# Performance work log

Hardware: AMD Instinct MI355X
Metric: run time of the kernel (lower is better)

## Reference

```python
import jax, jax.numpy as jnp
import numpy as np

N_NODES = 50000
N_EDGES = 600000
IN_CH = 300
HID = 128
N_CLASSES = 2
N_GRAPHS = 128
BN_EPS = 1e-5


def setup_inputs() -> dict:
    key = jax.random.key(0)
    ks = jax.random.split(key, 24)
    x = jax.random.normal(ks[0], (N_NODES, IN_CH), dtype=jnp.float32)
    edge_index = jax.random.randint(ks[1], (2, N_EDGES), 0, N_NODES, dtype=jnp.int64)
    batch = jnp.sort(jax.random.randint(ks[2], (N_NODES,), 0, N_GRAPHS, dtype=jnp.int64))

    def glorot(k, shape):
        fan_in, fan_out = shape
        s = jnp.sqrt(2.0 / (fan_in + fan_out)).astype(jnp.float32)
        return jax.random.normal(k, shape, dtype=jnp.float32) * s

    inp = {"x": x, "edge_index": edge_index, "batch": batch}
    # SAGEConv params: W_l (neighbor branch), W_r (root branch), bias
    dims = [(IN_CH, HID), (HID, HID), (HID, HID)]
    for i, (din, dout) in enumerate(dims, start=1):
        inp[f"W{i}l"] = glorot(ks[3 * i], (din, dout))
        inp[f"W{i}r"] = glorot(ks[3 * i + 1], (din, dout))
        inp[f"b{i}"] = jnp.zeros((dout,), dtype=jnp.float32)
        inp[f"g{i}"] = jnp.ones((dout,), dtype=jnp.float32)   # BN gamma
        inp[f"be{i}"] = jnp.zeros((dout,), dtype=jnp.float32)  # BN beta
    inp["Wc"] = glorot(ks[20], (HID, N_CLASSES))
    inp["bc"] = jnp.zeros((N_CLASSES,), dtype=jnp.float32)
    return inp


def _sage_conv(x, src, dst, Wl, Wr, b):
    # mean-aggregate neighbor features (messages flow src -> dst)
    msg_sum = jax.ops.segment_sum(x[src], dst, num_segments=N_NODES)
    deg = jax.ops.segment_sum(jnp.ones((src.shape[0],), dtype=x.dtype), dst,
                              num_segments=N_NODES)
    mean = msg_sum / jnp.maximum(deg, 1.0)[:, None]
    return mean @ Wl + x @ Wr + b


def _bn_relu(h, gamma, beta):
    mu = jnp.mean(h, axis=0)
    var = jnp.var(h, axis=0)
    h = (h - mu) * jax.lax.rsqrt(var + BN_EPS) * gamma + beta
    return jax.nn.relu(h)


def reference(x, edge_index, batch,
              W1l, W1r, b1, g1, be1,
              W2l, W2r, b2, g2, be2,
              W3l, W3r, b3, g3, be3,
              Wc, bc):
    src, dst = edge_index[0], edge_index[1]
    h = _bn_relu(_sage_conv(x, src, dst, W1l, W1r, b1), g1, be1)
    h = _bn_relu(_sage_conv(h, src, dst, W2l, W2r, b2), g2, be2)
    h = _bn_relu(_sage_conv(h, src, dst, W3l, W3r, b3), g3, be3)
    # global mean pool per graph
    pooled = jax.ops.segment_sum(h, batch, num_segments=N_GRAPHS)
    cnt = jax.ops.segment_sum(jnp.ones((h.shape[0],), dtype=h.dtype), batch,
                              num_segments=N_GRAPHS)
    hg = pooled / jnp.maximum(cnt, 1.0)[:, None]
    out = hg @ Wc + bc
    return out, hg
```

## Files before the change

kernel.cpp:

```cpp
#include <hip/hip_runtime.h>

#define N_NODES   50000
#define N_EDGES   600000
#define IN_CH     300
#define HID       128
#define N_CLASSES 2
#define N_GRAPHS  128
#define BN_EPS    1e-5f

#define NB ((N_NODES + 511) / 512)
#define KP1 320
#define NREP 32
#define DEGB ((N_EDGES + 255) / 256)

typedef __attribute__((ext_vector_type(8))) short bf8_t;
typedef __attribute__((ext_vector_type(4))) float f4_t;

__device__ __forceinline__ unsigned short f2bf(float x) {
    union { float f; unsigned u; } q; q.f = x;
    unsigned r = q.u + 0x7fffu + ((q.u >> 16) & 1u);
    return (unsigned short)(r >> 16);
}
__device__ __forceinline__ float bf2f(unsigned short h) {
    union { float f; unsigned u; } q; q.u = ((unsigned)h) << 16; return q.f;
}

__global__ __launch_bounds__(256) void deg_prepw(const int* __restrict__ dst,
                                                 int* __restrict__ ideg,
                                                 const float* __restrict__ W1l,
                                                 const float* __restrict__ W1r,
                                                 const float* __restrict__ W2l,
                                                 const float* __restrict__ W2r,
                                                 const float* __restrict__ W3l,
                                                 const float* __restrict__ W3r,
                                                 unsigned short* __restrict__ B1h,
                                                 unsigned short* __restrict__ B1l,
                                                 unsigned short* __restrict__ B2h,
                                                 unsigned short* __restrict__ B2l,
                                                 unsigned short* __restrict__ B3h,
                                                 unsigned short* __restrict__ B3l) {
    int b = blockIdx.x;
    if (b < DEGB) {
        int e = b * 256 + threadIdx.x;
        if (e < N_EDGES) atomicAdd(&ideg[dst[e]], 1);
        return;
    }
    int pb = b - DEGB;
    int layer, base;
    if (pb < 320)      { layer = 0; base = pb; }
    else if (pb < 448) { layer = 1; base = pb - 320; }
    else               { layer = 2; base = pb - 448; }
    int Kp = (layer == 0) ? KP1 : HID;
    int K  = (layer == 0) ? IN_CH : HID;
    const float* Wl = (layer == 0) ? W1l : ((layer == 1) ? W2l : W3l);
    const float* Wr = (layer == 0) ? W1r : ((layer == 1) ? W2r : W3r);
    unsigned short* Bh = (layer == 0) ? B1h : ((layer == 1) ? B2h : B3h);
    unsigned short* Bl = (layer == 0) ? B1l : ((layer == 1) ? B2l : B3l);
    int idx = base * 256 + threadIdx.x;
    int n = idx / Kp;
    int k = idx - n * Kp;
    float v = 0.f;
    if (k < K) v = (n < 128) ? Wl[k * 128 + n] : Wr[k * 128 + (n - 128)];
    unsigned short h = f2bf(v);
    unsigned short l = f2bf(v - bf2f(h));
    int NST   = Kp >> 5;
    int ntile = n >> 4;
    int l16n  = n & 15;
    int kstep = k >> 5;
    int kk    = k & 31;
    int lane2 = (kk >> 3) * 16 + l16n;
    int addr  = ((ntile * NST + kstep) * 64 + lane2) * 8 + (kk & 7);
    Bh[addr] = h;
    Bl[addr] = l;
}

__global__ __launch_bounds__(256) void scan_fused(const int* __restrict__ ideg,
                                                  int* __restrict__ row_start,
                                                  float* __restrict__ invdeg,
                                                  int* __restrict__ bsum,
                                                  int* __restrict__ bflag) {
    int b = blockIdx.x, t = threadIdx.x;
    int lane = t & 63, wv = t >> 6;
    int i0 = b * 512 + t * 2;
    int v0 = 0, v1 = 0;
    if (i0 < N_NODES) {
        int2 v = *(const int2*)&ideg[i0];
        v0 = v.x; v1 = v.y;
    }
    int tot = v0 + v1;
    int s = tot;
#pragma unroll
    for (int d = 1; d < 64; d <<= 1) {
        int u = __shfl_up(s, d);
        if (lane >= d) s += u;
    }
    __shared__ int ws[4];
    if (lane == 63) ws[wv] = s;
    __syncthreads();
    int btot = ws[0] + ws[1] + ws[2] + ws[3];
    if (t == 0) {
        atomicExch(&bsum[b], btot);
        __threadfence();
        atomicExch(&bflag[b], 1);
    }
    int part = 0;
    if (t < b) {
        while (atomicAdd(&bflag[t], 0) == 0) {}
        part = atomicAdd(&bsum[t], 0);
    }
#pragma unroll
    for (int d = 1; d < 64; d <<= 1) part += __shfl_down(part, d);
    __shared__ int ps[4];
    if (lane == 0) ps[wv] = part;
    __syncthreads();
    int boff = ps[0] + ps[1] + ps[2] + ps[3];
    int woff = 0;
    for (int w = 0; w < wv; ++w) woff += ws[w];
    int base = boff + woff + (s - tot);
    if (i0 < N_NODES) {
        row_start[i0]     = base;
        row_start[i0 + 1] = base + v0;
        invdeg[i0]     = 1.0f / fmaxf((float)v0, 1.0f);
        invdeg[i0 + 1] = 1.0f / fmaxf((float)v1, 1.0f);
    }
    if (t == 0 && b == NB - 1) row_start[N_NODES] = boff + btot;
}

__global__ __launch_bounds__(256) void fill_kernel(const int* __restrict__ src,
                                                   const int* __restrict__ dst,
                                                   const int* __restrict__ row_start,
                                                   int* __restrict__ cursor,
                                                   int* __restrict__ csr_src) {
    int e = blockIdx.x * 256 + threadIdx.x;
    if (e >= N_EDGES) return;
    int d = dst[e];
    int pos = row_start[d] + atomicAdd(&cursor[d], 1);
    csr_src[pos] = src[e];
}

__global__ __launch_bounds__(256) void gemm_mfma_x(const float* __restrict__ X,
                                                   int M,
                                                   const unsigned short* __restrict__ Bhi,
                                                   const unsigned short* __restrict__ Blo,
                                                   const float* __restrict__ bias,
                                                   unsigned short* __restrict__ C0,
                                                   float* __restrict__ C1) {
    __shared__ __align__(16) unsigned short sAh[2][64 * 32];
    __shared__ __align__(16) unsigned short sAl[2][64 * 32];

    const int tid  = threadIdx.x;
    const int lane = tid & 63;
    const int wave = tid >> 6;
    const int l16  = lane & 15;
    const int quad = lane >> 4;
    const long m0  = (long)blockIdx.x * 64;
    const int  n0  = wave * 64;

    f4_t acc[4][4];
#pragma unroll
    for (int mt = 0; mt < 4; ++mt)
#pragma unroll
        for (int nt = 0; nt < 4; ++nt) acc[mt][nt] = (f4_t){0.f, 0.f, 0.f, 0.f};

    const int ar  = tid >> 2;
    const int cl  = tid & 3;
    const int cpa = cl ^ ((ar >> 1) & 3);
    long agr = m0 + ar;
    if (agr >= M) agr = M - 1;
    const float* gX = X + agr * IN_CH;

    const int rsw = (quad ^ ((l16 >> 1) & 3)) * 8;
    const int NT  = KP1 / 32;

    const bf8_t* Bh0 = (const bf8_t*)Bhi;
    const bf8_t* Bl0 = (const bf8_t*)Blo;

    auto loadA = [&](int k0, float4& a0, float4& a1) {
        int gk = k0 + cl * 8;
        a0 = (gk + 4 <= IN_CH) ? *(const float4*)(gX + gk)
                               : make_float4(0.f, 0.f, 0.f, 0.f);
        a1 = (gk + 8 <= IN_CH) ? *(const float4*)(gX + gk + 4)
                               : make_float4(0.f, 0.f, 0.f, 0.f);
    };
    auto storeA = [&](int buf, float4 a0, float4 a1) {
        float f[8];
        f[0] = a0.x; f[1] = a0.y; f[2] = a0.z; f[3] = a0.w;
        f[4] = a1.x; f[5] = a1.y; f[6] = a1.z; f[7] = a1.w;
        bf8_t h8, l8;
#pragma unroll
        for (int j = 0; j < 8; ++j) {
            unsigned short h = f2bf(f[j]);
            h8[j] = (short)h;
            l8[j] = (short)f2bf(f[j] - bf2f(h));
        }
        *(bf8_t*)&sAh[buf][ar * 32 + cpa * 8] = h8;
        *(bf8_t*)&sAl[buf][ar * 32 + cpa * 8] = l8;
    };
    auto loadB = [&](int t, bf8_t (&bh)[4], bf8_t (&bl)[4]) {
#pragma unroll
        for (int nt = 0; nt < 4; ++nt) {
            long bi = ((long)(wave * 4 + nt) * NT + t) * 64 + lane;
            bh[nt] = Bh0[bi];
            bl[nt] = Bl0[bi];
        }
    };

    bf8_t bhv[4], blv[4];
    {
        float4 a0, a1;
        loadA(0, a0, a1);
        loadB(0, bhv, blv);
        storeA(0, a0, a1);
    }
    __syncthreads();

    int cur = 0;
    for (int t = 0; t < NT; ++t) {
        float4 na0 = make_float4(0.f, 0.f, 0.f, 0.f);
        float4 na1 = make_float4(0.f, 0.f, 0.f, 0.f);
        bf8_t nbh[4], nbl[4];
        const bool more = (t + 1 < NT);
        if (more) {
            loadA((t + 1) * 32, na0, na1);
            loadB(t + 1, nbh, nbl);
        }

        bf8_t ah[4], al[4];
#pragma unroll
        for (int mt = 0; mt < 4; ++mt) {
            ah[mt] = *(const bf8_t*)&sAh[cur][(mt * 16 + l16) * 32 + rsw];
            al[mt] = *(const bf8_t*)&sAl[cur][(mt * 16 + l16) * 32 + rsw];
        }
#pragma unroll
        for (int nt = 0; nt < 4; ++nt)
#pragma unroll
            for (int mt = 0; mt < 4; ++mt)
                acc[mt][nt] = __builtin_amdgcn_mfma_f32_16x16x32_bf16(ah[mt], bhv[nt], acc[mt][nt], 0, 0, 0);
#pragma unroll
        for (int nt = 0; nt < 4; ++nt)
#pragma unroll
            for (int mt = 0; mt < 4; ++mt)
                acc[mt][nt] = __builtin_amdgcn_mfma_f32_16x16x32_bf16(al[mt], bhv[nt], acc[mt][nt], 0, 0, 0);
#pragma unroll
        for (int nt = 0; nt < 4; ++nt)
#pragma unroll
            for (int mt = 0; mt < 4; ++mt)
                acc[mt][nt] = __builtin_amdgcn_mfma_f32_16x16x32_bf16(ah[mt], blv[nt], acc[mt][nt], 0, 0, 0);

        if (more) {
            storeA(cur ^ 1, na0, na1);
#pragma unroll
            for (int nt = 0; nt < 4; ++nt) {
                bhv[nt] = nbh[nt];
                blv[nt] = nbl[nt];
            }
        }
        __syncthreads();
        cur ^= 1;
    }

    const bool left = (n0 < 128);
    if (left) {
        int ncol[4];
#pragma unroll
        for (int nt = 0; nt < 4; ++nt) ncol[nt] = n0 + nt * 16 + l16;
#pragma unroll
        for (int mt = 0; mt < 4; ++mt)
#pragma unroll
            for (int r = 0; r < 4; ++r) {
                long row = m0 + mt * 16 + quad * 4 + r;
                if (row < M) {
#pragma unroll
                    for (int nt = 0; nt < 4; ++nt)
                        C0[row * 128 + ncol[nt]] = f2bf(acc[mt][nt][r]);
                }
            }
    } else {
        float badd[4];
        int   ncol[4];
#pragma unroll
        for (int nt = 0; nt < 4; ++nt) {
            int ng = n0 + nt * 16 + l16 - 128;
            ncol[nt] = ng;
            badd[nt] = bias[ng];
        }
#pragma unroll
        for (int mt = 0; mt < 4; ++mt)
#pragma unroll
            for (int r = 0; r < 4; ++r) {
                long row = m0 + mt * 16 + quad * 4 + r;
                if (row < M) {
#pragma unroll
                    for (int nt = 0; nt < 4; ++nt)
                        C1[row * 128 + ncol[nt]] = acc[mt][nt][r] + badd[nt];
                }
            }
    }
}

__global__ __launch_bounds__(256) void gemm_mfma_h(const float* __restrict__ Hpre,
                                                   int M,
                                                   const float* __restrict__ rep,
                                                   const float* __restrict__ gamma,
                                                   const float* __restrict__ beta,
                                                   const unsigned short* __restrict__ Bhi,
                                                   const unsigned short* __restrict__ Blo,
                                                   const float* __restrict__ bias,
                                                   unsigned short* __restrict__ C0,
                                                   float* __restrict__ C1) {
    __shared__ __align__(16) unsigned short sAh[2][64 * 32];
    __shared__ __align__(16) unsigned short sAl[2][64 * 32];
    __shared__ float sSC[256];

    const int tid  = threadIdx.x;
    const int lane = tid & 63;
    const int wave = tid >> 6;
    const int l16  = lane & 15;
    const int quad = lane >> 4;
    const long m0  = (long)blockIdx.x * 64;
    const int  n0  = wave * 64;

    {
        float* S = (float*)sAh;
        float a = 0.f;
#pragma unroll
        for (int r = 0; r < NREP; ++r) a += rep[r * 256 + tid];
        S[tid] = a;
        __syncthreads();
        if (tid < HID) {
            const float invn = 1.0f / (float)N_NODES;
            float mu  = S[tid] * invn;
            float var = S[HID + tid] * invn - mu * mu;
            float sc  = gamma[tid] * rsqrtf(var + BN_EPS);
            sSC[tid]       = sc;
            sSC[HID + tid] = beta[tid] - mu * sc;
        }
        __syncthreads();
    }

    f4_t acc[4][4];
#pragma unroll
    for (int mt = 0; mt < 4; ++mt)
#pragma unroll
        for (int nt = 0; nt < 4; ++nt) acc[mt][nt] = (f4_t){0.f, 0.f, 0.f, 0.f};

    const int ar  = tid >> 2;
    const int cl  = tid & 3;
    const int cpa = cl ^ ((ar >> 1) & 3);
    long agr = m0 + ar;
    if (agr >= M) agr = M - 1;
    const float* gH = Hpre + agr * HID;

    const int rsw = (quad ^ ((l16 >> 1) & 3)) * 8;
    const int NT  = HID / 32;

    const bf8_t* Bh0 = (const bf8_t*)Bhi;
    const bf8_t* Bl0 = (const bf8_t*)Blo;

    auto loadA = [&](int k0, float4& a0, float4& a1) {
        int gk = k0 + cl * 8;
        a0 = *(const float4*)(gH + gk);
        a1 = *(const float4*)(gH + gk + 4);
    };
    auto storeA = [&](int buf, int k0, float4 v0, float4 v1) {
        const int gk = k0 + cl * 8;
        float4 s0 = *(const float4*)&sSC[gk];
        float4 s1 = *(const float4*)&sSC[gk + 4];
        float4 t0 = *(const float4*)&sSC[HID + gk];
        float4 t1 = *(const float4*)&sSC[HID + gk + 4];
        float f[8];
        f[0] = fmaxf(v0.x * s0.x + t0.x, 0.f);
        f[1] = fmaxf(v0.y * s0.y + t0.y, 0.f);
        f[2] = fmaxf(v0.z * s0.z + t0.z, 0.f);
        f[3] = fmaxf(v0.w * s0.w + t0.w, 0.f);
        f[4] = fmaxf(v1.x * s1.x + t1.x, 0.f);
        f[5] = fmaxf(v1.y * s1.y + t1.y, 0.f);
        f[6] = fmaxf(v1.z * s1.z + t1.z, 0.f);
        f[7] = fmaxf(v1.w * s1.w + t1.w, 0.f);
        bf8_t h8, l8;
#pragma unroll
        for (int j = 0; j < 8; ++j) {
            unsigned short h = f2bf(f[j]);
            h8[j] = (short)h;
            l8[j] = (short)f2bf(f[j] - bf2f(h));
        }
        *(bf8_t*)&sAh[buf][ar * 32 + cpa * 8] = h8;
        *(bf8_t*)&sAl[buf][ar * 32 + cpa * 8] = l8;
    };
    auto loadB = [&](int t, bf8_t (&bh)[4], bf8_t (&bl)[4]) {
#pragma unroll
        for (int nt = 0; nt < 4; ++nt) {
            long bi = ((long)(wave * 4 + nt) * NT + t) * 64 + lane;
            bh[nt] = Bh0[bi];
            bl[nt] = Bl0[bi];
        }
    };

    bf8_t bhv[4], blv[4];
    {
        float4 a0, a1;
        loadA(0, a0, a1);
        loadB(0, bhv, blv);
        storeA(0, 0, a0, a1);
    }
    __syncthreads();

    int cur = 0;
#pragma unroll
    for (int t = 0; t < 4; ++t) {
        float4 na0 = make_float4(0.f, 0.f, 0.f, 0.f);
        float4 na1 = make_float4(0.f, 0.f, 0.f, 0.f);
        bf8_t nbh[4], nbl[4];
        const bool more = (t < 3);
        if (more) {
            loadA((t + 1) * 32, na0, na1);
            loadB(t + 1, nbh, nbl);
        }

        bf8_t ah[4], al[4];
#pragma unroll
        for (int mt = 0; mt < 4; ++mt) {
            ah[mt] = *(const bf8_t*)&sAh[cur][(mt * 16 + l16) * 32 + rsw];
            al[mt] = *(const bf8_t*)&sAl[cur][(mt * 16 + l16) * 32 + rsw];
        }
#pragma unroll
        for (int nt = 0; nt < 4; ++nt)
#pragma unroll
            for (int mt = 0; mt < 4; ++mt)
                acc[mt][nt] = __builtin_amdgcn_mfma_f32_16x16x32_bf16(ah[mt], bhv[nt], acc[mt][nt], 0, 0, 0);
#pragma unroll
        for (int nt = 0; nt < 4; ++nt)
#pragma unroll
            for (int mt = 0; mt < 4; ++mt)
                acc[mt][nt] = __builtin_amdgcn_mfma_f32_16x16x32_bf16(al[mt], bhv[nt], acc[mt][nt], 0, 0, 0);
#pragma unroll
        for (int nt = 0; nt < 4; ++nt)
#pragma unroll
            for (int mt = 0; mt < 4; ++mt)
                acc[mt][nt] = __builtin_amdgcn_mfma_f32_16x16x32_bf16(ah[mt], blv[nt], acc[mt][nt], 0, 0, 0);

        if (more) {
            storeA(cur ^ 1, (t + 1) * 32, na0, na1);
#pragma unroll
            for (int nt = 0; nt < 4; ++nt) {
                bhv[nt] = nbh[nt];
                blv[nt] = nbl[nt];
            }
        }
        __syncthreads();
        cur ^= 1;
    }

    const bool left = (n0 < 128);
    if (left) {
        int ncol[4];
#pragma unroll
        for (int nt = 0; nt < 4; ++nt) ncol[nt] = n0 + nt * 16 + l16;
#pragma unroll
        for (int mt = 0; mt < 4; ++mt)
#pragma unroll
            for (int r = 0; r < 4; ++r) {
                long row = m0 + mt * 16 + quad * 4 + r;
                if (row < M) {
#pragma unroll
                    for (int nt = 0; nt < 4; ++nt)
                        C0[row * 128 + ncol[nt]] = f2bf(acc[mt][nt][r]);
                }
            }
    } else {
        float badd[4];
        int   ncol[4];
#pragma unroll
        for (int nt = 0; nt < 4; ++nt) {
            int ng = n0 + nt * 16 + l16 - 128;
            ncol[nt] = ng;
            badd[nt] = bias[ng];
        }
#pragma unroll
        for (int mt = 0; mt < 4; ++mt)
#pragma unroll
            for (int r = 0; r < 4; ++r) {
                long row = m0 + mt * 16 + quad * 4 + r;
                if (row < M) {
#pragma unroll
                    for (int nt = 0; nt < 4; ++nt)
                        C1[row * 128 + ncol[nt]] = acc[mt][nt][r] + badd[nt];
                }
            }
    }
}

__global__ __launch_bounds__(256) void gather_agg(const unsigned short* __restrict__ Pl,
                                                  const int* __restrict__ row_start,
                                                  const int* __restrict__ csr_src,
                                                  const float* __restrict__ invdeg,
                                                  float* __restrict__ out,
                                                  float* __restrict__ rep) {
    int slot = threadIdx.x >> 5;
    int lane = threadIdx.x & 31;
    int node = blockIdx.x * 8 + slot;
    int beg = row_start[node];
    int end = row_start[node + 1];
    const unsigned short* base = Pl + lane * 4;
    float sx = 0.f, sy = 0.f, sz = 0.f, sw = 0.f;
    int j = beg;
    int deg = end - beg;

    if (deg > 0) {
        int n16 = (deg < 16) ? deg : 16;
        int idx[16];
#pragma unroll
        for (int u = 0; u < 16; ++u)
            idx[u] = csr_src[(u < n16) ? (j + u) : j];
        ushort4 v[16];
#pragma unroll
        for (int u = 0; u < 16; ++u)
            v[u] = *(const ushort4*)(base + (long)idx[u] * HID);
#pragma unroll
        for (int u = 0; u < 16; ++u) {
            float m = (u < n16) ? 1.f : 0.f;
            sx += m * bf2f(v[u].x); sy += m * bf2f(v[u].y);
            sz += m * bf2f(v[u].z); sw += m * bf2f(v[u].w);
        }
        j += n16;
    }
    for (; j + 8 <= end; j += 8) {
        int idx[8];
#pragma unroll
        for (int u = 0; u < 8; ++u) idx[u] = csr_src[j + u];
        ushort4 v[8];
#pragma unroll
        for (int u = 0; u < 8; ++u) v[u] = *(const ushort4*)(base + (long)idx[u] * HID);
#pragma unroll
        for (int u = 0; u < 8; ++u) {
            sx += bf2f(v[u].x); sy += bf2f(v[u].y);
            sz += bf2f(v[u].z); sw += bf2f(v[u].w);
        }
    }
    if (j + 4 <= end) {
        int idx[4];
#pragma unroll
        for (int u = 0; u < 4; ++u) idx[u] = csr_src[j + u];
        ushort4 v[4];
#pragma unroll
        for (int u = 0; u < 4; ++u) v[u] = *(const ushort4*)(base + (long)idx[u] * HID);
#pragma unroll
        for (int u = 0; u < 4; ++u) {
            sx += bf2f(v[u].x); sy += bf2f(v[u].y);
            sz += bf2f(v[u].z); sw += bf2f(v[u].w);
        }
        j += 4;
    }
    for (; j < end; ++j) {
        int i0 = csr_src[j];
        ushort4 v0 = *(const ushort4*)(base + (long)i0 * HID);
        sx += bf2f(v0.x); sy += bf2f(v0.y); sz += bf2f(v0.z); sw += bf2f(v0.w);
    }
    float w = invdeg[node];
    float* o = out + (long)node * HID + lane * 4;
    float4 cur = *(float4*)o;
    cur.x += sx * w;
    cur.y += sy * w;
    cur.z += sz * w;
    cur.w += sw * w;
    *(float4*)o = cur;

    __shared__ float red[8][HID];
    float* repb = rep + (blockIdx.x & (NREP - 1)) * 256;
    *(float4*)&red[slot][lane * 4] = make_float4(cur.x, cur.y, cur.z, cur.w);
    __syncthreads();
    if (threadIdx.x < HID) {
        float tsum = 0.f;
#pragma unroll
        for (int s = 0; s < 8; ++s) tsum += red[s][threadIdx.x];
        atomicAdd(&repb[threadIdx.x], tsum);
    }
    __syncthreads();
    *(float4*)&red[slot][lane * 4] = make_float4(cur.x * cur.x, cur.y * cur.y,
                                                 cur.z * cur.z, cur.w * cur.w);
    __syncthreads();
    if (threadIdx.x < HID) {
        float tsum = 0.f;
#pragma unroll
        for (int s = 0; s < 8; ++s) tsum += red[s][threadIdx.x];
        atomicAdd(&repb[HID + threadIdx.x], tsum);
    }
}

__global__ __launch_bounds__(1024) void poolhead_bn(const float* __restrict__ h,
                                                    const int* __restrict__ batch,
                                                    const float* __restrict__ rep,
                                                    const float* __restrict__ gamma,
                                                    const float* __restrict__ beta,
                                                    const float* __restrict__ Wc,
                                                    const float* __restrict__ bc,
                                                    float* __restrict__ out) {
    __shared__ float S[256];
    __shared__ float SC[256];
    int g = blockIdx.x;
    int t = threadIdx.x;
    int c = t & 127;
    int half = t >> 7;
    if (t < 256) {
        float a = 0.f;
#pragma unroll
        for (int r = 0; r < NREP; ++r) a += rep[r * 256 + t];
        S[t] = a;
    }
    __shared__ int lo_sh, hi_sh;
    if (t == 0) {
        int lo = 0, hi = N_NODES;
        while (lo < hi) { int m = (lo + hi) >> 1; if (batch[m] < g) lo = m + 1; else hi = m; }
        lo_sh = lo;
        int lo2 = lo, hi2 = N_NODES;
        while (lo2 < hi2) { int m = (lo2 + hi2) >> 1; if (batch[m] < g + 1) lo2 = m + 1; else hi2 = m; }
        hi_sh = lo2;
    }
    __syncthreads();
    if (t < HID) {
        const float invn = 1.0f / (float)N_NODES;
        float mu  = S[t] * invn;
        float var = S[HID + t] * invn - mu * mu;
        float sc  = gamma[t] * rsqrtf(var + BN_EPS);
        SC[t]       = sc;
        SC[HID + t] = beta[t] - mu * sc;
    }
    __syncthreads();
    float bsc = SC[c], bsh = SC[HID + c];
    int lo = lo_sh, hi = hi_sh;
    float a0 = 0.f, a1 = 0.f, a2 = 0.f, a3 = 0.f;
    int r = lo + half;
    for (; r + 24 < hi; r += 32) {
        a0 += fmaxf(h[(long)(r +  0) * HID + c] * bsc + bsh, 0.f);
        a1 += fmaxf(h[(long)(r +  8) * HID + c] * bsc + bsh, 0.f);
        a2 += fmaxf(h[(long)(r + 16) * HID + c] * bsc + bsh, 0.f);
        a3 += fmaxf(h[(long)(r + 24) * HID + c] * bsc + bsh, 0.f);
    }
    for (; r < hi; r += 8) a0 += fmaxf(h[(long)r * HID + c] * bsc + bsh, 0.f);
    __shared__ float red[8][HID];
    red[half][c] = (a0 + a1) + (a2 + a3);
    __syncthreads();
    __shared__ float r0[HID], r1[HID];
    if (t < HID) {
        float inv = 1.0f / fmaxf((float)(hi - lo), 1.0f);
        float v = 0.f;
#pragma unroll
        for (int s = 0; s < 8; ++s) v += red[s][t];
        v *= inv;
        out[N_GRAPHS * N_CLASSES + g * HID + t] = v;
        r0[t] = v * Wc[t * 2 + 0];
        r1[t] = v * Wc[t * 2 + 1];
    }
    __syncthreads();
    if (t < 2) {
        const float* rr = t ? r1 : r0;
        float sum = bc[t];
        for (int i = 0; i < HID; ++i) sum += rr[i];
        out[g * 2 + t] = sum;
    }
}

extern "C" void kernel_launch(void* const* d_in, const int* in_sizes, int n_in,
                              void* d_out, int out_size, void* d_ws, size_t ws_size,
                              hipStream_t stream) {
    const float* x     = (const float*)d_in[0];
    const int*   ei    = (const int*)d_in[1];
    const int*   batch = (const int*)d_in[2];
    const float* W1l = (const float*)d_in[3];
    const float* W1r = (const float*)d_in[4];
    const float* b1  = (const float*)d_in[5];
    const float* g1  = (const float*)d_in[6];
    const float* be1 = (const float*)d_in[7];
    const float* W2l = (const float*)d_in[8];
    const float* W2r = (const float*)d_in[9];
    const float* b2  = (const float*)d_in[10];
    const float* g2  = (const float*)d_in[11];
    const float* be2 = (const float*)d_in[12];
    const float* W3l = (const float*)d_in[13];
    const float* W3r = (const float*)d_in[14];
    const float* b3  = (const float*)d_in[15];
    const float* g3  = (const float*)d_in[16];
    const float* be3 = (const float*)d_in[17];
    const float* Wc  = (const float*)d_in[18];
    const float* bc  = (const float*)d_in[19];

    const int* src = ei;
    const int* dst = ei + N_EDGES;

    float* ws = (float*)d_ws;
    const long FEAT = (long)N_NODES * HID;
    unsigned short* Pl16 = (unsigned short*)ws;
    float* buf1 = ws + FEAT;
    float* buf2 = ws + 2 * FEAT;
    int*   ideg      = (int*)(ws + 3 * FEAT);
    int*   cursor    = ideg + N_NODES;
    int*   bsum      = cursor + N_NODES;
    int*   bflag     = bsum + 128;
    int*   row_start = bflag + 128;
    int*   csr_src   = row_start + N_NODES + 4;
    float* invdeg    = (float*)(csr_src + N_EDGES);
    float* reps      = invdeg + N_NODES;
    unsigned short* B1h = (unsigned short*)(reps + 3 * NREP * 256);
    unsigned short* B1l = B1h + 256 * KP1;
    unsigned short* B2h = B1l + 256 * KP1;
    unsigned short* B2l = B2h + 256 * HID;
    unsigned short* B3h = B2l + 256 * HID;
    unsigned short* B3l = B3h + 256 * HID;

    float* outp = (float*)d_out;

    const int gemm_grid   = (N_NODES + 63) / 64;
    const int gather_grid = N_NODES / 8;
    const int dp_grid     = DEGB + 320 + 128 + 128;

    hipMemsetAsync(ideg, 0, (2 * N_NODES + 256) * sizeof(int), stream);
    hipMemsetAsync(reps, 0, 3 * NREP * 256 * sizeof(float), stream);

    deg_prepw<<<dp_grid, 256, 0, stream>>>(dst, ideg, W1l, W1r, W2l, W2r, W3l, W3r,
                                           B1h, B1l, B2h, B2l, B3h, B3l);
    scan_fused<<<NB, 256, 0, stream>>>(ideg, row_start, invdeg, bsum, bflag);
    fill_kernel<<<(N_EDGES + 255) / 256, 256, 0, stream>>>(src, dst, row_start, cursor, csr_src);

    gemm_mfma_x<<<gemm_grid, 256, 0, stream>>>(x, N_NODES, B1h, B1l, b1, Pl16, buf1);
    gather_agg<<<gather_grid, 256, 0, stream>>>(Pl16, row_start, csr_src, invdeg, buf1, reps);

    gemm_mfma_h<<<gemm_grid, 256, 0, stream>>>(buf1, N_NODES, reps, g1, be1,
                                               B2h, B2l, b2, Pl16, buf2);
    gather_agg<<<gather_grid, 256, 0, stream>>>(Pl16, row_start, csr_src, invdeg, buf2, reps + NREP * 256);

    gemm_mfma_h<<<gemm_grid, 256, 0, stream>>>(buf2, N_NODES, reps + NREP * 256, g2, be2,
                                               B3h, B3l, b3, Pl16, buf1);
    gather_agg<<<gather_grid, 256, 0, stream>>>(Pl16, row_start, csr_src, invdeg, buf1, reps + 2 * NREP * 256);

    poolhead_bn<<<N_GRAPHS, 1024, 0, stream>>>(buf1, batch, reps + 2 * NREP * 256,
                                               g3, be3, Wc, bc, outp);
}
```

Measured before the change: 371.1 us.

## Stage full A tile in LDS upfront and halve row tile for first GEMM

Both MFMA GEMM kernels now load and convert the entire K extent of their A row tile into shared memory in one up-front phase, replacing the per-K-step double-buffered load/convert/sync pipeline. The loop then only prefetches B fragments and issues MFMAs, with no barriers inside it. The x-input GEMM also shrinks its row tile from 64 to 32 rows, doubling its grid, to keep LDS usage modest and add parallelism. The cost is that global loads no longer overlap with compute inside a block. Overlap now has to come from other resident blocks, and the 32-row tile halves B reuse per block.

Measured after the change: 374.4 us. Within noise of the previous version (+0.9%).

```diff
diff --git a/kernel.cpp b/kernel.cpp
--- a/kernel.cpp
+++ b/kernel.cpp
@@ -145,57 +145,67 @@
                                                    const float* __restrict__ bias,
                                                    unsigned short* __restrict__ C0,
                                                    float* __restrict__ C1) {
-    __shared__ __align__(16) unsigned short sAh[2][64 * 32];
-    __shared__ __align__(16) unsigned short sAl[2][64 * 32];
+    __shared__ __align__(16) unsigned short sAh[10 * 1024];
+    __shared__ __align__(16) unsigned short sAl[10 * 1024];
 
     const int tid  = threadIdx.x;
     const int lane = tid & 63;
     const int wave = tid >> 6;
     const int l16  = lane & 15;
     const int quad = lane >> 4;
-    const long m0  = (long)blockIdx.x * 64;
+    const long m0  = (long)blockIdx.x * 32;
     const int  n0  = wave * 64;
 
-    f4_t acc[4][4];
-#pragma unroll
-    for (int mt = 0; mt < 4; ++mt)
+    f4_t acc[2][4];
+#pragma unroll
+    for (int mt = 0; mt < 2; ++mt)
 #pragma unroll
         for (int nt = 0; nt < 4; ++nt) acc[mt][nt] = (f4_t){0.f, 0.f, 0.f, 0.f};
 
-    const int ar  = tid >> 2;
-    const int cl  = tid & 3;
-    const int cpa = cl ^ ((ar >> 1) & 3);
-    long agr = m0 + ar;
-    if (agr >= M) agr = M - 1;
-    const float* gX = X + agr * IN_CH;
+    {
+        const int ar  = tid >> 3;
+        const int sub = tid & 7;
+        long agr = m0 + ar;
+        if (agr >= M) agr = M - 1;
+        const float* gX = X + agr * IN_CH;
+        const int swm = (ar >> 1) & 3;
+        float4 va[5][2];
+#pragma unroll
+        for (int i = 0; i < 5; ++i) {
+            int c  = sub + 8 * i;
+            int gk = c * 8;
+            va[i][0] = (gk + 4 <= IN_CH) ? *(const float4*)(gX + gk)
+                                         : make_float4(0.f, 0.f, 0.f, 0.f);
+            va[i][1] = (gk + 8 <= IN_CH) ? *(const float4*)(gX + gk + 4)
+                                         : make_float4(0.f, 0.f, 0.f, 0.f);
+        }
+#pragma unroll
+        for (int i = 0; i < 5; ++i) {
+            int c     = sub + 8 * i;
+            int kstep = c >> 2;
+            int cpa   = (c & 3) ^ swm;
+            float f[8];
+            f[0] = va[i][0].x; f[1] = va[i][0].y; f[2] = va[i][0].z; f[3] = va[i][0].w;
+            f[4] = va[i][1].x; f[5] = va[i][1].y; f[6] = va[i][1].z; f[7] = va[i][1].w;
+            bf8_t h8, l8;
+#pragma unroll
+            for (int j = 0; j < 8; ++j) {
+                unsigned short h = f2bf(f[j]);
+                h8[j] = (short)h;
+                l8[j] = (short)f2bf(f[j] - bf2f(h));
+            }
+            int idx = kstep * 1024 + ar * 32 + cpa * 8;
+            *(bf8_t*)&sAh[idx] = h8;
+            *(bf8_t*)&sAl[idx] = l8;
+        }
+    }
+    __syncthreads();
 
     const int rsw = (quad ^ ((l16 >> 1) & 3)) * 8;
     const int NT  = KP1 / 32;
-
     const bf8_t* Bh0 = (const bf8_t*)Bhi;
     const bf8_t* Bl0 = (const bf8_t*)Blo;
 
-    auto loadA = [&](int k0, float4& a0, float4& a1) {
-        int gk = k0 + cl * 8;
-        a0 = (gk + 4 <= IN_CH) ? *(const float4*)(gX + gk)
-                               : make_float4(0.f, 0.f, 0.f, 0.f);
-        a1 = (gk + 8 <= IN_CH) ? *(const float4*)(gX + gk + 4)
-                               : make_float4(0.f, 0.f, 0.f, 0.f);
-    };
-    auto storeA = [&](int buf, float4 a0, float4 a1) {
-        float f[8];
-        f[0] = a0.x; f[1] = a0.y; f[2] = a0.z; f[3] = a0.w;
-        f[4] = a1.x; f[5] = a1.y; f[6] = a1.z; f[7] = a1.w;
-        bf8_t h8, l8;
-#pragma unroll
-        for (int j = 0; j < 8; ++j) {
-            unsigned short h = f2bf(f[j]);
-            h8[j] = (short)h;
-            l8[j] = (short)f2bf(f[j] - bf2f(h));
-        }
-        *(bf8_t*)&sAh[buf][ar * 32 + cpa * 8] = h8;
-        *(bf8_t*)&sAl[buf][ar * 32 + cpa * 8] = l8;
-    };
     auto loadB = [&](int t, bf8_t (&bh)[4], bf8_t (&bl)[4]) {
 #pragma unroll
         for (int nt = 0; nt < 4; ++nt) {
@@ -206,57 +216,42 @@
     };
 
     bf8_t bhv[4], blv[4];
-    {
-        float4 a0, a1;
-        loadA(0, a0, a1);
-        loadB(0, bhv, blv);
-        storeA(0, a0, a1);
-    }
-    __syncthreads();
-
-    int cur = 0;
+    loadB(0, bhv, blv);
     for (int t = 0; t < NT; ++t) {
-        float4 na0 = make_float4(0.f, 0.f, 0.f, 0.f);
-        float4 na1 = make_float4(0.f, 0.f, 0.f, 0.f);
         bf8_t nbh[4], nbl[4];
         const bool more = (t + 1 < NT);
+        if (more) loadB(t + 1, nbh, nbl);
+
+        bf8_t ah[2], al[2];
+#pragma unroll
+        for (int mt = 0; mt < 2; ++mt) {
+            int idx = t * 1024 + (mt * 16 + l16) * 32 + rsw;
+            ah[mt] = *(const bf8_t*)&sAh[idx];
+            al[mt] = *(const bf8_t*)&sAl[idx];
+        }
+#pragma unroll
+        for (int nt = 0; nt < 4; ++nt)
+#pragma unroll
+            for (int mt = 0; mt < 2; ++mt)
+                acc[mt][nt] = __builtin_amdgcn_mfma_f32_16x16x32_bf16(ah[mt], bhv[nt], acc[mt][nt], 0, 0, 0);
+#pragma unroll
+        for (int nt = 0; nt < 4; ++nt)
+#pragma unroll
+            for (int mt = 0; mt < 2; ++mt)
+                acc[mt][nt] = __builtin_amdgcn_mfma_f32_16x16x32_bf16(al[mt], bhv[nt], acc[mt][nt], 0, 0, 0);
+#pragma unroll
+        for (int nt = 0; nt < 4; ++nt)
+#pragma unroll
+            for (int mt = 0; mt < 2; ++mt)
+                acc[mt][nt] = __builtin_amdgcn_mfma_f32_16x16x32_bf16(ah[mt], blv[nt], acc[mt][nt], 0, 0, 0);
+
         if (more) {
-            loadA((t + 1) * 32, na0, na1);
-            loadB(t + 1, nbh, nbl);
-        }
-
-        bf8_t ah[4], al[4];
-#pragma unroll
-        for (int mt = 0; mt < 4; ++mt) {
-            ah[mt] = *(const bf8_t*)&sAh[cur][(mt * 16 + l16) * 32 + rsw];
-            al[mt] = *(const bf8_t*)&sAl[cur][(mt * 16 + l16) * 32 + rsw];
-        }
-#pragma unroll
-        for (int nt = 0; nt < 4; ++nt)
-#pragma unroll
-            for (int mt = 0; mt < 4; ++mt)
-                acc[mt][nt] = __builtin_amdgcn_mfma_f32_16x16x32_bf16(ah[mt], bhv[nt], acc[mt][nt], 0, 0, 0);
-#pragma unroll
-        for (int nt = 0; nt < 4; ++nt)
-#pragma unroll
-            for (int mt = 0; mt < 4; ++mt)
-                acc[mt][nt] = __builtin_amdgcn_mfma_f32_16x16x32_bf16(al[mt], bhv[nt], acc[mt][nt], 0, 0, 0);
-#pragma unroll
-        for (int nt = 0; nt < 4; ++nt)
-#pragma unroll
-            for (int mt = 0; mt < 4; ++mt)
-                acc[mt][nt] = __builtin_amdgcn_mfma_f32_16x16x32_bf16(ah[mt], blv[nt], acc[mt][nt], 0, 0, 0);
-
-        if (more) {
-            storeA(cur ^ 1, na0, na1);
 #pragma unroll
             for (int nt = 0; nt < 4; ++nt) {
                 bhv[nt] = nbh[nt];
                 blv[nt] = nbl[nt];
             }
         }
-        __syncthreads();
-        cur ^= 1;
     }
 
     const bool left = (n0 < 128);
@@ -265,7 +260,7 @@
 #pragma unroll
         for (int nt = 0; nt < 4; ++nt) ncol[nt] = n0 + nt * 16 + l16;
 #pragma unroll
-        for (int mt = 0; mt < 4; ++mt)
+        for (int mt = 0; mt < 2; ++mt)
 #pragma unroll
             for (int r = 0; r < 4; ++r) {
                 long row = m0 + mt * 16 + quad * 4 + r;
@@ -285,7 +280,7 @@
             badd[nt] = bias[ng];
         }
 #pragma unroll
-        for (int mt = 0; mt < 4; ++mt)
+        for (int mt = 0; mt < 2; ++mt)
 #pragma unroll
             for (int r = 0; r < 4; ++r) {
                 long row = m0 + mt * 16 + quad * 4 + r;
@@ -308,8 +303,8 @@
                                                    const float* __restrict__ bias,
                                                    unsigned short* __restrict__ C0,
                                                    float* __restrict__ C1) {
-    __shared__ __align__(16) unsigned short sAh[2][64 * 32];
-    __shared__ __align__(16) unsigned short sAl[2][64 * 32];
+    __shared__ __align__(16) unsigned short sAh[4 * 2048];
+    __shared__ __align__(16) unsigned short sAl[4 * 2048];
     __shared__ float sSC[256];
 
     const int tid  = threadIdx.x;
@@ -344,49 +339,58 @@
 #pragma unroll
         for (int nt = 0; nt < 4; ++nt) acc[mt][nt] = (f4_t){0.f, 0.f, 0.f, 0.f};
 
-    const int ar  = tid >> 2;
-    const int cl  = tid & 3;
-    const int cpa = cl ^ ((ar >> 1) & 3);
-    long agr = m0 + ar;
-    if (agr >= M) agr = M - 1;
-    const float* gH = Hpre + agr * HID;
+    {
+        const int ar = tid >> 2;
+        const int cl = tid & 3;
+        long agr = m0 + ar;
+        if (agr >= M) agr = M - 1;
+        const float* gH = Hpre + agr * HID;
+        const int swm = (ar >> 1) & 3;
+        float4 va[4][2];
+#pragma unroll
+        for (int i = 0; i < 4; ++i) {
+            int gk = (cl + 4 * i) * 8;
+            va[i][0] = *(const float4*)(gH + gk);
+            va[i][1] = *(const float4*)(gH + gk + 4);
+        }
+#pragma unroll
+        for (int i = 0; i < 4; ++i) {
+            int c     = cl + 4 * i;
+            int kstep = c >> 2;
+            int cpa   = (c & 3) ^ swm;
+            int gk    = c * 8;
+            float4 s0 = *(const float4*)&sSC[gk];
+            float4 s1 = *(const float4*)&sSC[gk + 4];
+            float4 t0 = *(const float4*)&sSC[HID + gk];
+            float4 t1 = *(const float4*)&sSC[HID + gk + 4];
+            float f[8];
+            f[0] = fmaxf(va[i][0].x * s0.x + t0.x, 0.f);
+            f[1] = fmaxf(va[i][0].y * s0.y + t0.y, 0.f);
+            f[2] = fmaxf(va[i][0].z * s0.z + t0.z, 0.f);
+            f[3] = fmaxf(va[i][0].w * s0.w + t0.w, 0.f);
+            f[4] = fmaxf(va[i][1].x * s1.x + t1.x, 0.f);
+            f[5] = fmaxf(va[i][1].y * s1.y + t1.y, 0.f);
+            f[6] = fmaxf(va[i][1].z * s1.z + t1.z, 0.f);
+            f[7] = fmaxf(va[i][1].w * s1.w + t1.w, 0.f);
+            bf8_t h8, l8;
+#pragma unroll
+            for (int j = 0; j < 8; ++j) {
+                unsigned short h = f2bf(f[j]);
+                h8[j] = (short)h;
+                l8[j] = (short)f2bf(f[j] - bf2f(h));
+            }
+            int idx = kstep * 2048 + ar * 32 + cpa * 8;
+            *(bf8_t*)&sAh[idx] = h8;
+            *(bf8_t*)&sAl[idx] = l8;
+        }
+    }
+    __syncthreads();
 
     const int rsw = (quad ^ ((l16 >> 1) & 3)) * 8;
     const int NT  = HID / 32;
-
     const bf8_t* Bh0 = (const bf8_t*)Bhi;
     const bf8_t* Bl0 = (const bf8_t*)Blo;
 
-    auto loadA = [&](int k0, float4& a0, float4& a1) {
-        int gk = k0 + cl * 8;
-        a0 = *(const float4*)(gH + gk);
-        a1 = *(const float4*)(gH + gk + 4);
-    };
-    auto storeA = [&](int buf, int k0, float4 v0, float4 v1) {
-        const int gk = k0 + cl * 8;
-        float4 s0 = *(const float4*)&sSC[gk];
-        float4 s1 = *(const float4*)&sSC[gk + 4];
-        float4 t0 = *(const float4*)&sSC[HID + gk];
-        float4 t1 = *(const float4*)&sSC[HID + gk + 4];
-        float f[8];
-        f[0] = fmaxf(v0.x * s0.x + t0.x, 0.f);
-        f[1] = fmaxf(v0.y * s0.y + t0.y, 0.f);
-        f[2] = fmaxf(v0.z * s0.z + t0.z, 0.f);
-        f[3] = fmaxf(v0.w * s0.w + t0.w, 0.f);
-        f[4] = fmaxf(v1.x * s1.x + t1.x, 0.f);
-        f[5] = fmaxf(v1.y * s1.y + t1.y, 0.f);
-        f[6] = fmaxf(v1.z * s1.z + t1.z, 0.f);
-        f[7] = fmaxf(v1.w * s1.w + t1.w, 0.f);
-        bf8_t h8, l8;
-#pragma unroll
-        for (int j = 0; j < 8; ++j) {
-            unsigned short h = f2bf(f[j]);
-            h8[j] = (short)h;
-            l8[j] = (short)f2bf(f[j] - bf2f(h));
-        }
-        *(bf8_t*)&sAh[buf][ar * 32 + cpa * 8] = h8;
-        *(bf8_t*)&sAl[buf][ar * 32 + cpa * 8] = l8;
-    };
     auto loadB = [&](int t, bf8_t (&bh)[4], bf8_t (&bl)[4]) {
 #pragma unroll
         for (int nt = 0; nt < 4; ++nt) {
@@ -397,31 +401,19 @@
     };
 
     bf8_t bhv[4], blv[4];
-    {
-        float4 a0, a1;
-        loadA(0, a0, a1);
-        loadB(0, bhv, blv);
-        storeA(0, 0, a0, a1);
-    }
-    __syncthreads();
-
-    int cur = 0;
+    loadB(0, bhv, blv);
 #pragma unroll
     for (int t = 0; t < 4; ++t) {
-        float4 na0 = make_float4(0.f, 0.f, 0.f, 0.f);
-        float4 na1 = make_float4(0.f, 0.f, 0.f, 0.f);
         bf8_t nbh[4], nbl[4];
         const bool more = (t < 3);
-        if (more) {
-            loadA((t + 1) * 32, na0, na1);
-            loadB(t + 1, nbh, nbl);
-        }
+        if (more) loadB(t + 1, nbh, nbl);
 
         bf8_t ah[4], al[4];
 #pragma unroll
         for (int mt = 0; mt < 4; ++mt) {
-            ah[mt] = *(const bf8_t*)&sAh[cur][(mt * 16 + l16) * 32 + rsw];
-            al[mt] = *(const bf8_t*)&sAl[cur][(mt * 16 + l16) * 32 + rsw];
+            int idx = t * 2048 + (mt * 16 + l16) * 32 + rsw;
+            ah[mt] = *(const bf8_t*)&sAh[idx];
+            al[mt] = *(const bf8_t*)&sAl[idx];
         }
 #pragma unroll
         for (int nt = 0; nt < 4; ++nt)
@@ -440,15 +432,12 @@
                 acc[mt][nt] = __builtin_amdgcn_mfma_f32_16x16x32_bf16(ah[mt], blv[nt], acc[mt][nt], 0, 0, 0);
 
         if (more) {
-            storeA(cur ^ 1, (t + 1) * 32, na0, na1);
 #pragma unroll
             for (int nt = 0; nt < 4; ++nt) {
                 bhv[nt] = nbh[nt];
                 blv[nt] = nbl[nt];
             }
         }
-        __syncthreads();
-        cur ^= 1;
     }
 
     const bool left = (n0 < 128);
@@ -709,7 +698,8 @@
 
     float* outp = (float*)d_out;
 
-    const int gemm_grid   = (N_NODES + 63) / 64;
+    const int gemmx_grid  = (N_NODES + 31) / 32;
+    const int gemmh_grid  = (N_NODES + 63) / 64;
     const int gather_grid = N_NODES / 8;
     const int dp_grid     = DEGB + 320 + 128 + 128;
 
@@ -721,15 +711,15 @@
     scan_fused<<<NB, 256, 0, stream>>>(ideg, row_start, invdeg, bsum, bflag);
     fill_kernel<<<(N_EDGES + 255) / 256, 256, 0, stream>>>(src, dst, row_start, cursor, csr_src);
 
-    gemm_mfma_x<<<gemm_grid, 256, 0, stream>>>(x, N_NODES, B1h, B1l, b1, Pl16, buf1);
+    gemm_mfma_x<<<gemmx_grid, 256, 0, stream>>>(x, N_NODES, B1h, B1l, b1, Pl16, buf1);
     gather_agg<<<gather_grid, 256, 0, stream>>>(Pl16, row_start, csr_src, invdeg, buf1, reps);
 
-    gemm_mfma_h<<<gemm_grid, 256, 0, stream>>>(buf1, N_NODES, reps, g1, be1,
-                                               B2h, B2l, b2, Pl16, buf2);
+    gemm_mfma_h<<<gemmh_grid, 256, 0, stream>>>(buf1, N_NODES, reps, g1, be1,
+                                                B2h, B2l, b2, Pl16, buf2);
     gather_agg<<<gather_grid, 256, 0, stream>>>(Pl16, row_start, csr_src, invdeg, buf2, reps + NREP * 256);
 
-    gemm_mfma_h<<<gemm_grid, 256, 0, stream>>>(buf2, N_NODES, reps + NREP * 256, g2, be2,
-                                               B3h, B3l, b3, Pl16, buf1);
+    gemm_mfma_h<<<gemmh_grid, 256, 0, stream>>>(buf2, N_NODES, reps + NREP * 256, g2, be2,
+                                                B3h, B3l, b3, Pl16, buf1);
     gather_agg<<<gather_grid, 256, 0, stream>>>(Pl16, row_start, csr_src, invdeg, buf1, reps + 2 * NREP * 256);
 
     poolhead_bn<<<N_GRAPHS, 1024, 0, stream>>>(buf1, batch, reps + 2 * NREP * 256,
```

## Fuse CSR fill into first GEMM launch and merge BN stat reductions

Applied to the files above, without the earlier changes.

Appends the edge-to-CSR fill blocks to the layer-1 GEMM grid, so the fill runs concurrently with the GEMM instead of as its own launch. Also computes sum and sum-of-squares in a single shared-memory reduction pass in gather_agg, which drops two barriers and one shared write. The fused kernel carries the GEMM's shared-memory footprint for the fill blocks too, which may limit occupancy for those blocks.

Result: faster. 356.6 us (median of 3 runs) (-3.9%).

```diff
diff --git a/kernel.cpp b/kernel.cpp
--- a/kernel.cpp
+++ b/kernel.cpp
@@ -12,6 +12,8 @@
 #define KP1 320
 #define NREP 32
 #define DEGB ((N_EDGES + 255) / 256)
+#define GEMMX_BLOCKS ((N_NODES + 63) / 64)
+#define FILLB ((N_EDGES + 255) / 256)
 
 typedef __attribute__((ext_vector_type(8))) short bf8_t;
 typedef __attribute__((ext_vector_type(4))) float f4_t;
@@ -126,25 +128,28 @@
     if (t == 0 && b == NB - 1) row_start[N_NODES] = boff + btot;
 }
 
-__global__ __launch_bounds__(256) void fill_kernel(const int* __restrict__ src,
-                                                   const int* __restrict__ dst,
-                                                   const int* __restrict__ row_start,
-                                                   int* __restrict__ cursor,
-                                                   int* __restrict__ csr_src) {
-    int e = blockIdx.x * 256 + threadIdx.x;
-    if (e >= N_EDGES) return;
-    int d = dst[e];
-    int pos = row_start[d] + atomicAdd(&cursor[d], 1);
-    csr_src[pos] = src[e];
-}
-
-__global__ __launch_bounds__(256) void gemm_mfma_x(const float* __restrict__ X,
+__global__ __launch_bounds__(256) void gemm_x_fill(const float* __restrict__ X,
                                                    int M,
                                                    const unsigned short* __restrict__ Bhi,
                                                    const unsigned short* __restrict__ Blo,
                                                    const float* __restrict__ bias,
                                                    unsigned short* __restrict__ C0,
-                                                   float* __restrict__ C1) {
+                                                   float* __restrict__ C1,
+                                                   const int* __restrict__ esrc,
+                                                   const int* __restrict__ edst,
+                                                   const int* __restrict__ row_start,
+                                                   int* __restrict__ cursor,
+                                                   int* __restrict__ csr_src) {
+    if (blockIdx.x >= GEMMX_BLOCKS) {
+        int e = (blockIdx.x - GEMMX_BLOCKS) * 256 + threadIdx.x;
+        if (e < N_EDGES) {
+            int d = edst[e];
+            int pos = row_start[d] + atomicAdd(&cursor[d], 1);
+            csr_src[pos] = esrc[e];
+        }
+        return;
+    }
+
     __shared__ __align__(16) unsigned short sAh[2][64 * 32];
     __shared__ __align__(16) unsigned short sAl[2][64 * 32];
 
@@ -570,20 +575,15 @@
     *(float4*)&red[slot][lane * 4] = make_float4(cur.x, cur.y, cur.z, cur.w);
     __syncthreads();
     if (threadIdx.x < HID) {
-        float tsum = 0.f;
-#pragma unroll
-        for (int s = 0; s < 8; ++s) tsum += red[s][threadIdx.x];
+        float tsum = 0.f, tsq = 0.f;
+#pragma unroll
+        for (int s = 0; s < 8; ++s) {
+            float v = red[s][threadIdx.x];
+            tsum += v;
+            tsq  += v * v;
+        }
         atomicAdd(&repb[threadIdx.x], tsum);
-    }
-    __syncthreads();
-    *(float4*)&red[slot][lane * 4] = make_float4(cur.x * cur.x, cur.y * cur.y,
-                                                 cur.z * cur.z, cur.w * cur.w);
-    __syncthreads();
-    if (threadIdx.x < HID) {
-        float tsum = 0.f;
-#pragma unroll
-        for (int s = 0; s < 8; ++s) tsum += red[s][threadIdx.x];
-        atomicAdd(&repb[HID + threadIdx.x], tsum);
+        atomicAdd(&repb[HID + threadIdx.x], tsq);
     }
 }
 
@@ -710,6 +710,7 @@
     float* outp = (float*)d_out;
 
     const int gemm_grid   = (N_NODES + 63) / 64;
+    const int gxf_grid    = GEMMX_BLOCKS + FILLB;
     const int gather_grid = N_NODES / 8;
     const int dp_grid     = DEGB + 320 + 128 + 128;
 
@@ -719,9 +720,9 @@
     deg_prepw<<<dp_grid, 256, 0, stream>>>(dst, ideg, W1l, W1r, W2l, W2r, W3l, W3r,
                                            B1h, B1l, B2h, B2l, B3h, B3l);
     scan_fused<<<NB, 256, 0, stream>>>(ideg, row_start, invdeg, bsum, bflag);
-    fill_kernel<<<(N_EDGES + 255) / 256, 256, 0, stream>>>(src, dst, row_start, cursor, csr_src);
-
-    gemm_mfma_x<<<gemm_grid, 256, 0, stream>>>(x, N_NODES, B1h, B1l, b1, Pl16, buf1);
+
+    gemm_x_fill<<<gxf_grid, 256, 0, stream>>>(x, N_NODES, B1h, B1l, b1, Pl16, buf1,
+                                              src, dst, row_start, cursor, csr_src);
     gather_agg<<<gather_grid, 256, 0, stream>>>(Pl16, row_start, csr_src, invdeg, buf1, reps);
 
     gemm_mfma_h<<<gemm_grid, 256, 0, stream>>>(buf1, N_NODES, reps, g1, be1,
```
